# Kernel tuning notes

Measured on AMD Instinct MI355X. Metric: run time of the kernel, lower is better.

The kernel has to match this reference:

```python
import jax, jax.numpy as jnp
import numpy as np

B, LC, LQ, D = 256, 400, 50, 128
NEG = 1e12


def setup_inputs() -> dict:
    key = jax.random.key(0)
    ks = jax.random.split(key, 7)
    return {
        "x_cont": jax.random.normal(ks[0], (B, LC, D), dtype=jnp.float32),
        "x_ques": jax.random.normal(ks[1], (B, LQ, D), dtype=jnp.float32),
        "W0": jax.random.normal(ks[2], (D, 1), dtype=jnp.float32) * (1.0 / np.sqrt(D)),
        "W1": jax.random.normal(ks[3], (D, 1), dtype=jnp.float32) * (1.0 / np.sqrt(D)),
        "W2": jax.random.normal(ks[4], (1, 1, D), dtype=jnp.float32) * (1.0 / np.sqrt(D)),
        "cont_len": jax.random.randint(ks[5], (B, 1), 1, LC, dtype=jnp.int32),
        "ques_len": jax.random.randint(ks[6], (B, 1), 1, LQ, dtype=jnp.int32),
    }


def reference(x_cont, x_ques, W0, W1, W2, cont_len, ques_len):
    # Trilinear similarity S[b,c,q] = xc.W0 + xq.W1 + (xc*W2).xq
    s_c = x_cont @ W0                                   # (B, LC, 1)
    s_q = jnp.swapaxes(x_ques @ W1, 1, 2)               # (B, 1, LQ)
    s_f = jnp.einsum('bcd,bqd->bcq', x_cont * W2, x_ques)
    S = s_c + s_q + s_f                                 # (B, LC, LQ)

    # Length masks: position valid iff pos < seq_len (matches one_hot+cumsum)
    q_mask = (jnp.arange(LQ)[None, :] < ques_len).astype(S.dtype)  # (B, LQ)
    c_mask = (jnp.arange(LC)[None, :] < cont_len).astype(S.dtype)  # (B, LC)

    S_bar = jax.nn.softmax(S - (1.0 - q_mask)[:, None, :] * NEG, axis=-1)
    S_T = jnp.swapaxes(
        jax.nn.softmax(S - (1.0 - c_mask)[:, :, None] * NEG, axis=1), 1, 2)  # (B, LQ, LC)

    c2q = S_bar @ x_ques                                # (B, LC, D)
    q2c = (S_bar @ S_T) @ x_cont                        # (B, LC, D)

    result = jnp.concatenate(
        [x_cont, c2q, x_cont * c2q, x_cont * q2c], axis=-1)  # (B, LC, 4D)
    return result, S_bar, S_T
```

## Files before the change

### kernel.cpp

```cpp
#include <hip/hip_runtime.h>
#include <math.h>

#define B 256
#define LC 400
#define LQ 50
#define D 128
#define CT 64

__global__ __launch_bounds__(256) void k_scores_softmax(
    const float* __restrict__ xc_g, const float* __restrict__ xq_g,
    const float* __restrict__ W0, const float* __restrict__ W1,
    const float* __restrict__ W2, const int* __restrict__ cont_len,
    const int* __restrict__ ques_len,
    float* __restrict__ S_bar, float* __restrict__ S_T)
{
    __shared__ float sS[LC * 51];
    __shared__ __align__(16) float xq[56 * 132];
    __shared__ __align__(16) float xc[64 * 132];
    __shared__ float w[3 * D];
    __shared__ float scT[64];
    __shared__ float sq[56];
    __shared__ float rowmax[LC], rowinv[LC];
    __shared__ float colmax[LQ], colinv[LQ];
    __shared__ float red[256];

    const int b = blockIdx.x;
    const int t = threadIdx.x;
    const int clen = cont_len[b];
    const int qlen = ques_len[b];

    const float4* xq4g = (const float4*)(xq_g + (size_t)b * LQ * D);
    for (int i = t; i < LQ * 32; i += 256)
        ((float4*)xq)[(i >> 5) * 33 + (i & 31)] = xq4g[i];
    {
        const float4* g0 = (const float4*)(xc_g + (size_t)b * LC * D);
        for (int i = t; i < 64 * 32; i += 256)
            ((float4*)xc)[(i >> 5) * 33 + (i & 31)] = g0[i];
    }
    if (t < D) { w[t] = W0[t]; w[D + t] = W1[t]; w[2 * D + t] = W2[t]; }
    __syncthreads();

    if (t < LQ) {
        const float4* r = (const float4*)(xq + t * 132);
        const float4* wv = (const float4*)(w + D);
        float4 a = {0.f, 0.f, 0.f, 0.f};
#pragma unroll
        for (int d = 0; d < 32; ++d) {
            float4 u = r[d], v = wv[d];
            a.x += u.x * v.x; a.y += u.y * v.y; a.z += u.z * v.z; a.w += u.w * v.w;
        }
        sq[t] = a.x + a.y + a.z + a.w;
    }
    __syncthreads();
    for (int i = t; i < LQ * D; i += 256)
        xq[(i >> 7) * 132 + (i & 127)] *= w[2 * D + (i & 127)];
    __syncthreads();

    const int qg = t & 7;
    const int cg = (t >> 3) & 15;

    for (int tile = 0; tile < 7; ++tile) {
        const int c0 = tile * 64;
        const int nc = min(64, LC - c0);

        float4 pf[8];
        const int c0n = c0 + 64;
        const int ncn = (tile < 6) ? min(64, LC - c0n) : 0;
        const float4* gn = (const float4*)(xc_g + ((size_t)b * LC + c0n) * D);
#pragma unroll
        for (int k = 0; k < 8; ++k) {
            const int i = t + k * 256;
            if (i < ncn * 32) pf[k] = gn[i];
        }

        float acc[4][7];
        if (t < 128) {
#pragma unroll
            for (int i = 0; i < 4; ++i)
#pragma unroll
                for (int j = 0; j < 7; ++j) acc[i][j] = 0.f;
            const float4* xc4 = (const float4*)xc;
            const float4* xq4 = (const float4*)xq;
#pragma unroll 4
            for (int d4 = 0; d4 < 32; ++d4) {
                const float4 a0 = xc4[(cg + 0)  * 33 + d4];
                const float4 a1 = xc4[(cg + 16) * 33 + d4];
                const float4 a2 = xc4[(cg + 32) * 33 + d4];
                const float4 a3 = xc4[(cg + 48) * 33 + d4];
#pragma unroll
                for (int j = 0; j < 7; ++j) {
                    const float4 bq = xq4[(qg * 7 + j) * 33 + d4];
                    acc[0][j] += a0.x*bq.x + a0.y*bq.y + a0.z*bq.z + a0.w*bq.w;
                    acc[1][j] += a1.x*bq.x + a1.y*bq.y + a1.z*bq.z + a1.w*bq.w;
                    acc[2][j] += a2.x*bq.x + a2.y*bq.y + a2.z*bq.z + a2.w*bq.w;
                    acc[3][j] += a3.x*bq.x + a3.y*bq.y + a3.z*bq.z + a3.w*bq.w;
                }
            }
        } else if (t < 192) {
            const int c = t - 128;
            if (c < nc) {
                const float4* r = (const float4*)(xc + c * 132);
                const float4* wv = (const float4*)w;
                float4 a = {0.f, 0.f, 0.f, 0.f};
#pragma unroll
                for (int d = 0; d < 32; ++d) {
                    float4 u = r[d], v = wv[d];
                    a.x += u.x*v.x; a.y += u.y*v.y; a.z += u.z*v.z; a.w += u.w*v.w;
                }
                scT[c] = a.x + a.y + a.z + a.w;
            }
        }
        __syncthreads();

        if (t < 128) {
#pragma unroll
            for (int i = 0; i < 4; ++i) {
                const int c = cg + 16 * i;
                if (c < nc) {
                    const float sc_c = scT[c];
#pragma unroll
                    for (int j = 0; j < 7; ++j) {
                        const int q = qg * 7 + j;
                        if (q < LQ) sS[(c0 + c) * 51 + q] = acc[i][j] + sc_c + sq[q];
                    }
                }
            }
        }
#pragma unroll
        for (int k = 0; k < 8; ++k) {
            const int i = t + k * 256;
            if (i < ncn * 32) ((float4*)xc)[(i >> 5) * 33 + (i & 31)] = pf[k];
        }
        __syncthreads();
    }

    const int qq_ = t % LQ;
    const int r_ = t / LQ;
    if (t < 250) {
        float m = -INFINITY;
        const int ce = min((r_ + 1) * 80, clen);
        for (int c = r_ * 80; c < ce; ++c) m = fmaxf(m, sS[c * 51 + qq_]);
        red[t] = m;
    }
    __syncthreads();
    if (t < LQ) {
        float m = red[t];
#pragma unroll
        for (int rr = 1; rr < 5; ++rr) m = fmaxf(m, red[rr * LQ + t]);
        colmax[t] = m;
    }
    __syncthreads();
    if (t < 250) {
        float s = 0.f;
        const float cm = colmax[qq_];
        const int ce = min((r_ + 1) * 80, clen);
        for (int c = r_ * 80; c < ce; ++c) s += __expf(sS[c * 51 + qq_] - cm);
        red[t] = s;
    }
    __syncthreads();
    if (t < LQ) {
        float s = red[t];
#pragma unroll
        for (int rr = 1; rr < 5; ++rr) s += red[rr * LQ + t];
        colinv[t] = 1.f / s;
    }
    for (int c = t; c < LC; c += 256) {
        float m = -INFINITY;
        for (int q = 0; q < qlen; ++q) m = fmaxf(m, sS[c * 51 + q]);
        float s = 0.f;
        for (int q = 0; q < qlen; ++q) s += __expf(sS[c * 51 + q] - m);
        rowmax[c] = m;
        rowinv[c] = 1.f / s;
    }
    __syncthreads();

    float* Sb = S_bar + (size_t)b * LC * LQ;
    for (int i = t; i < LC * LQ; i += 256) {
        const int c = i / LQ, q = i - c * LQ;
        Sb[i] = (q < qlen) ? __expf(sS[c * 51 + q] - rowmax[c]) * rowinv[c] : 0.f;
    }
    float* STb = S_T + (size_t)b * LQ * LC;
    for (int i = t; i < LQ * LC; i += 256) {
        const int q = i / LC, c = i - q * LC;
        STb[i] = (c < clen) ? __expf(sS[c * 51 + q] - colmax[q]) * colinv[q] : 0.f;
    }
}

__global__ __launch_bounds__(256) void k_qc(
    const float* __restrict__ S_T, const float* __restrict__ xc_g,
    float* __restrict__ T)
{
    __shared__ __align__(16) float sT[56 * 404];

    const int b = blockIdx.x;
    const int t = threadIdx.x;
    const float4* STb4 = (const float4*)(S_T + (size_t)b * LQ * LC);
    float4* sTw = (float4*)sT;
    for (int i = t; i < LQ * 100; i += 256)
        sTw[(i / 100) * 101 + (i % 100)] = STb4[i];
    __syncthreads();

    const int d4 = t & 31, qg = t >> 5;
    float4 acc[7];
#pragma unroll
    for (int j = 0; j < 7; ++j) acc[j] = make_float4(0.f, 0.f, 0.f, 0.f);

    const float4* xcv = (const float4*)xc_g + (size_t)b * LC * 32 + d4;
    const float4* sT4 = (const float4*)sT;
    for (int c = 0; c < LC; c += 4) {
        const float4 x0 = xcv[(c + 0) * 32];
        const float4 x1 = xcv[(c + 1) * 32];
        const float4 x2 = xcv[(c + 2) * 32];
        const float4 x3 = xcv[(c + 3) * 32];
#pragma unroll
        for (int j = 0; j < 7; ++j) {
            const float4 wv = sT4[(qg * 7 + j) * 101 + (c >> 2)];
            acc[j].x += wv.x * x0.x + wv.y * x1.x + wv.z * x2.x + wv.w * x3.x;
            acc[j].y += wv.x * x0.y + wv.y * x1.y + wv.z * x2.y + wv.w * x3.y;
            acc[j].z += wv.x * x0.z + wv.y * x1.z + wv.z * x2.z + wv.w * x3.z;
            acc[j].w += wv.x * x0.w + wv.y * x1.w + wv.z * x2.w + wv.w * x3.w;
        }
    }
    float4* Tb = (float4*)T + (size_t)b * LQ * 32 + d4;
#pragma unroll
    for (int j = 0; j < 7; ++j) {
        const int qq = qg * 7 + j;
        if (qq < LQ) Tb[qq * 32] = acc[j];
    }
}

#define FMA4(A, s, V) { A.x += (s) * V.x; A.y += (s) * V.y; A.z += (s) * V.z; A.w += (s) * V.w; }

__global__ __launch_bounds__(256) void k_out(
    const float* __restrict__ S_bar, const float* __restrict__ xq_g,
    const float* __restrict__ Tm, const float* __restrict__ xc_g,
    float* __restrict__ out)
{
    __shared__ __align__(16) float xqL[LQ * 132];
    __shared__ __align__(16) float TL[LQ * 132];
    __shared__ __align__(16) float sbT[LQ * 68];

    const int b = blockIdx.y;
    const int c0 = blockIdx.x * CT;
    const int t = threadIdx.x;
    const int nc = min(CT, LC - c0);

    const float4* xq4g = (const float4*)(xq_g + (size_t)b * LQ * D);
    const float4* T4g  = (const float4*)(Tm + (size_t)b * LQ * D);
    for (int i = t; i < LQ * 32; i += 256) {
        const int row = i >> 5, col = i & 31;
        ((float4*)xqL)[row * 33 + col] = xq4g[i];
        ((float4*)TL)[row * 33 + col]  = T4g[i];
    }
    const float* sb_g = S_bar + (size_t)(b * LC + c0) * LQ;
    for (int i = t; i < nc * LQ; i += 256) {
        const int c = i / LQ, q = i - c * LQ;
        sbT[q * 68 + c] = sb_g[i];
    }
    __syncthreads();

    const int d4 = t & 31, cg = t >> 5;
    float4 c2q[8], q2c[8];
#pragma unroll
    for (int i = 0; i < 8; ++i) {
        c2q[i] = make_float4(0.f, 0.f, 0.f, 0.f);
        q2c[i] = make_float4(0.f, 0.f, 0.f, 0.f);
    }
    const float4* xq4 = (const float4*)xqL;
    const float4* T4  = (const float4*)TL;
    const float4* sb4 = (const float4*)sbT;
    const int cb2 = cg * 2;
    for (int qq = 0; qq < LQ; ++qq) {
        const float4 xv = xq4[qq * 33 + d4];
        const float4 tv = T4[qq * 33 + d4];
        const float4 s0 = sb4[qq * 17 + cb2];
        const float4 s1 = sb4[qq * 17 + cb2 + 1];
        FMA4(c2q[0], s0.x, xv); FMA4(q2c[0], s0.x, tv);
        FMA4(c2q[1], s0.y, xv); FMA4(q2c[1], s0.y, tv);
        FMA4(c2q[2], s0.z, xv); FMA4(q2c[2], s0.z, tv);
        FMA4(c2q[3], s0.w, xv); FMA4(q2c[3], s0.w, tv);
        FMA4(c2q[4], s1.x, xv); FMA4(q2c[4], s1.x, tv);
        FMA4(c2q[5], s1.y, xv); FMA4(q2c[5], s1.y, tv);
        FMA4(c2q[6], s1.z, xv); FMA4(q2c[6], s1.z, tv);
        FMA4(c2q[7], s1.w, xv); FMA4(q2c[7], s1.w, tv);
    }

    const int cbase = cg * 8;
    const float4* xcv = (const float4*)xc_g;
    float4* out4 = (float4*)out;
#pragma unroll
    for (int i = 0; i < 8; ++i) {
        const int c = cbase + i;
        if (c < nc) {
            const int row = b * LC + c0 + c;
            const float4 xc = xcv[(size_t)row * 32 + d4];
            float4* o = out4 + (size_t)row * 128 + d4;
            o[0] = xc;
            o[32] = c2q[i];
            o[64] = make_float4(xc.x * c2q[i].x, xc.y * c2q[i].y,
                                xc.z * c2q[i].z, xc.w * c2q[i].w);
            o[96] = make_float4(xc.x * q2c[i].x, xc.y * q2c[i].y,
                                xc.z * q2c[i].z, xc.w * q2c[i].w);
        }
    }
}

extern "C" void kernel_launch(void* const* d_in, const int* in_sizes, int n_in,
                              void* d_out, int out_size, void* d_ws, size_t ws_size,
                              hipStream_t stream)
{
    (void)in_sizes; (void)n_in; (void)out_size; (void)ws_size;
    const float* x_cont = (const float*)d_in[0];
    const float* x_ques = (const float*)d_in[1];
    const float* W0 = (const float*)d_in[2];
    const float* W1 = (const float*)d_in[3];
    const float* W2 = (const float*)d_in[4];
    const int* cont_len = (const int*)d_in[5];
    const int* ques_len = (const int*)d_in[6];

    float* out = (float*)d_out;
    float* out_res  = out;
    float* out_Sbar = out + (size_t)B * LC * 4 * D;
    float* out_ST   = out_Sbar + (size_t)B * LC * LQ;
    float* Tws = (float*)d_ws;

    k_scores_softmax<<<B, 256, 0, stream>>>(x_cont, x_ques, W0, W1, W2,
                                            cont_len, ques_len, out_Sbar, out_ST);
    k_qc<<<B, 256, 0, stream>>>(out_ST, x_cont, Tws);
    k_out<<<dim3(7, B), 256, 0, stream>>>(out_Sbar, x_ques, Tws, x_cont, out_res);
}
```

Measured before the change: 520.7 us.

## Split score kernel across context tiles and move column softmax into qc kernel

New measurement: 446.7 us. -14.2%, faster.

```diff
diff --git a/kernel.cpp b/kernel.cpp
--- a/kernel.cpp
+++ b/kernel.cpp
@@ -7,36 +7,31 @@
 #define D 128
 #define CT 64
 
-__global__ __launch_bounds__(256) void k_scores_softmax(
+__global__ __launch_bounds__(256) void k_scores_rowsm(
     const float* __restrict__ xc_g, const float* __restrict__ xq_g,
     const float* __restrict__ W0, const float* __restrict__ W1,
-    const float* __restrict__ W2, const int* __restrict__ cont_len,
-    const int* __restrict__ ques_len,
-    float* __restrict__ S_bar, float* __restrict__ S_T)
+    const float* __restrict__ W2, const int* __restrict__ ques_len,
+    float* __restrict__ S_bar, float* __restrict__ S_Traw)
 {
-    __shared__ float sS[LC * 51];
     __shared__ __align__(16) float xq[56 * 132];
-    __shared__ __align__(16) float xc[64 * 132];
+    __shared__ __align__(16) float xc[CT * 132];
     __shared__ float w[3 * D];
-    __shared__ float scT[64];
-    __shared__ float sq[56];
-    __shared__ float rowmax[LC], rowinv[LC];
-    __shared__ float colmax[LQ], colinv[LQ];
-    __shared__ float red[256];
-
-    const int b = blockIdx.x;
+    __shared__ float sq[56], sc[CT];
+    __shared__ float sS[CT * 51];
+    __shared__ float rowm[CT], rowi[CT];
+
+    const int b = blockIdx.y;
+    const int c0 = blockIdx.x * CT;
     const int t = threadIdx.x;
-    const int clen = cont_len[b];
+    const int nc = min(CT, LC - c0);
     const int qlen = ques_len[b];
 
     const float4* xq4g = (const float4*)(xq_g + (size_t)b * LQ * D);
     for (int i = t; i < LQ * 32; i += 256)
         ((float4*)xq)[(i >> 5) * 33 + (i & 31)] = xq4g[i];
-    {
-        const float4* g0 = (const float4*)(xc_g + (size_t)b * LC * D);
-        for (int i = t; i < 64 * 32; i += 256)
-            ((float4*)xc)[(i >> 5) * 33 + (i & 31)] = g0[i];
-    }
+    const float4* xc4g = (const float4*)(xc_g + (size_t)(b * LC + c0) * D);
+    for (int i = t; i < nc * 32; i += 256)
+        ((float4*)xc)[(i >> 5) * 33 + (i & 31)] = xc4g[i];
     if (t < D) { w[t] = W0[t]; w[D + t] = W1[t]; w[2 * D + t] = W2[t]; }
     __syncthreads();
 
@@ -50,160 +45,140 @@
             a.x += u.x * v.x; a.y += u.y * v.y; a.z += u.z * v.z; a.w += u.w * v.w;
         }
         sq[t] = a.x + a.y + a.z + a.w;
+    } else if (t >= 64 && t < 64 + CT) {
+        const int c = t - 64;
+        if (c < nc) {
+            const float4* r = (const float4*)(xc + c * 132);
+            const float4* wv = (const float4*)w;
+            float4 a = {0.f, 0.f, 0.f, 0.f};
+#pragma unroll
+            for (int d = 0; d < 32; ++d) {
+                float4 u = r[d], v = wv[d];
+                a.x += u.x * v.x; a.y += u.y * v.y; a.z += u.z * v.z; a.w += u.w * v.w;
+            }
+            sc[c] = a.x + a.y + a.z + a.w;
+        }
     }
     __syncthreads();
     for (int i = t; i < LQ * D; i += 256)
         xq[(i >> 7) * 132 + (i & 127)] *= w[2 * D + (i & 127)];
     __syncthreads();
 
-    const int qg = t & 7;
-    const int cg = (t >> 3) & 15;
-
-    for (int tile = 0; tile < 7; ++tile) {
-        const int c0 = tile * 64;
-        const int nc = min(64, LC - c0);
-
-        float4 pf[8];
-        const int c0n = c0 + 64;
-        const int ncn = (tile < 6) ? min(64, LC - c0n) : 0;
-        const float4* gn = (const float4*)(xc_g + ((size_t)b * LC + c0n) * D);
-#pragma unroll
-        for (int k = 0; k < 8; ++k) {
-            const int i = t + k * 256;
-            if (i < ncn * 32) pf[k] = gn[i];
-        }
-
-        float acc[4][7];
-        if (t < 128) {
-#pragma unroll
-            for (int i = 0; i < 4; ++i)
-#pragma unroll
-                for (int j = 0; j < 7; ++j) acc[i][j] = 0.f;
-            const float4* xc4 = (const float4*)xc;
-            const float4* xq4 = (const float4*)xq;
-#pragma unroll 4
-            for (int d4 = 0; d4 < 32; ++d4) {
-                const float4 a0 = xc4[(cg + 0)  * 33 + d4];
-                const float4 a1 = xc4[(cg + 16) * 33 + d4];
-                const float4 a2 = xc4[(cg + 32) * 33 + d4];
-                const float4 a3 = xc4[(cg + 48) * 33 + d4];
-#pragma unroll
-                for (int j = 0; j < 7; ++j) {
-                    const float4 bq = xq4[(qg * 7 + j) * 33 + d4];
-                    acc[0][j] += a0.x*bq.x + a0.y*bq.y + a0.z*bq.z + a0.w*bq.w;
-                    acc[1][j] += a1.x*bq.x + a1.y*bq.y + a1.z*bq.z + a1.w*bq.w;
-                    acc[2][j] += a2.x*bq.x + a2.y*bq.y + a2.z*bq.z + a2.w*bq.w;
-                    acc[3][j] += a3.x*bq.x + a3.y*bq.y + a3.z*bq.z + a3.w*bq.w;
-                }
+    const int qg = t & 7, cg = t >> 3;
+    const int cA = cg * 2;
+    if (cA < nc) {
+        float accA[7] = {0, 0, 0, 0, 0, 0, 0};
+        float accB[7] = {0, 0, 0, 0, 0, 0, 0};
+        const float4* xc4 = (const float4*)xc;
+        const float4* xq4 = (const float4*)xq;
+#pragma unroll 8
+        for (int d4 = 0; d4 < 32; ++d4) {
+            const float4 a0 = xc4[cA * 33 + d4];
+            const float4 a1 = xc4[(cA + 1) * 33 + d4];
+#pragma unroll
+            for (int j = 0; j < 7; ++j) {
+                const float4 bq = xq4[(qg * 7 + j) * 33 + d4];
+                accA[j] += a0.x * bq.x + a0.y * bq.y + a0.z * bq.z + a0.w * bq.w;
+                accB[j] += a1.x * bq.x + a1.y * bq.y + a1.z * bq.z + a1.w * bq.w;
             }
-        } else if (t < 192) {
-            const int c = t - 128;
-            if (c < nc) {
-                const float4* r = (const float4*)(xc + c * 132);
-                const float4* wv = (const float4*)w;
-                float4 a = {0.f, 0.f, 0.f, 0.f};
-#pragma unroll
-                for (int d = 0; d < 32; ++d) {
-                    float4 u = r[d], v = wv[d];
-                    a.x += u.x*v.x; a.y += u.y*v.y; a.z += u.z*v.z; a.w += u.w*v.w;
-                }
-                scT[c] = a.x + a.y + a.z + a.w;
+        }
+        const float scA = sc[cA], scB = sc[cA + 1];
+#pragma unroll
+        for (int j = 0; j < 7; ++j) {
+            const int q = qg * 7 + j;
+            if (q < LQ) {
+                sS[cA * 51 + q] = accA[j] + scA + sq[q];
+                sS[(cA + 1) * 51 + q] = accB[j] + scB + sq[q];
             }
         }
-        __syncthreads();
-
-        if (t < 128) {
-#pragma unroll
-            for (int i = 0; i < 4; ++i) {
-                const int c = cg + 16 * i;
-                if (c < nc) {
-                    const float sc_c = scT[c];
-#pragma unroll
-                    for (int j = 0; j < 7; ++j) {
-                        const int q = qg * 7 + j;
-                        if (q < LQ) sS[(c0 + c) * 51 + q] = acc[i][j] + sc_c + sq[q];
-                    }
-                }
-            }
-        }
-#pragma unroll
-        for (int k = 0; k < 8; ++k) {
-            const int i = t + k * 256;
-            if (i < ncn * 32) ((float4*)xc)[(i >> 5) * 33 + (i & 31)] = pf[k];
-        }
-        __syncthreads();
-    }
-
-    const int qq_ = t % LQ;
-    const int r_ = t / LQ;
+    }
+    __syncthreads();
+
+    if (t < nc) {
+        float m = -INFINITY;
+        for (int q = 0; q < qlen; ++q) m = fmaxf(m, sS[t * 51 + q]);
+        float s = 0.f;
+        for (int q = 0; q < qlen; ++q) s += __expf(sS[t * 51 + q] - m);
+        rowm[t] = m;
+        rowi[t] = 1.f / s;
+    }
+    __syncthreads();
+
+    float* Sb = S_bar + (size_t)(b * LC + c0) * LQ;
+    for (int i = t; i < nc * LQ; i += 256) {
+        const int c = i / LQ, q = i - c * LQ;
+        Sb[i] = (q < qlen) ? __expf(sS[c * 51 + q] - rowm[c]) * rowi[c] : 0.f;
+    }
+    float* STb = S_Traw + (size_t)b * LQ * LC + c0;
+    for (int i = t; i < LQ * 64; i += 256) {
+        const int q = i >> 6, c = i & 63;
+        if (c < nc) STb[q * LC + c] = sS[c * 51 + q];
+    }
+}
+
+__global__ __launch_bounds__(512) void k_colsm_qc(
+    float* __restrict__ S_T, const float* __restrict__ xc_g,
+    const int* __restrict__ cont_len, float* __restrict__ T)
+{
+    __shared__ __align__(16) float sT[56 * 404];
+    __shared__ float red[256];
+    __shared__ float colmax[LQ], colinv[LQ];
+
+    const int b = blockIdx.x;
+    const int t = threadIdx.x;
+    const int clen = cont_len[b];
+    float* STb = S_T + (size_t)b * LQ * LC;
+
+    const float4* STb4 = (const float4*)STb;
+    float4* sTw = (float4*)sT;
+    for (int i = t; i < LQ * 100; i += 512)
+        sTw[(i / 100) * 101 + (i % 100)] = STb4[i];
+    __syncthreads();
+
+    const int qr = t / 5, g = t - qr * 5;
     if (t < 250) {
         float m = -INFINITY;
-        const int ce = min((r_ + 1) * 80, clen);
-        for (int c = r_ * 80; c < ce; ++c) m = fmaxf(m, sS[c * 51 + qq_]);
+        const int ce = min((g + 1) * 80, clen);
+        for (int c = g * 80; c < ce; ++c) m = fmaxf(m, sT[qr * 404 + c]);
         red[t] = m;
     }
     __syncthreads();
     if (t < LQ) {
-        float m = red[t];
-#pragma unroll
-        for (int rr = 1; rr < 5; ++rr) m = fmaxf(m, red[rr * LQ + t]);
+        float m = red[t * 5];
+#pragma unroll
+        for (int k = 1; k < 5; ++k) m = fmaxf(m, red[t * 5 + k]);
         colmax[t] = m;
     }
     __syncthreads();
     if (t < 250) {
         float s = 0.f;
-        const float cm = colmax[qq_];
-        const int ce = min((r_ + 1) * 80, clen);
-        for (int c = r_ * 80; c < ce; ++c) s += __expf(sS[c * 51 + qq_] - cm);
+        const float cm = colmax[qr];
+        const int ce = min((g + 1) * 80, clen);
+        for (int c = g * 80; c < ce; ++c) s += __expf(sT[qr * 404 + c] - cm);
         red[t] = s;
     }
     __syncthreads();
     if (t < LQ) {
-        float s = red[t];
-#pragma unroll
-        for (int rr = 1; rr < 5; ++rr) s += red[rr * LQ + t];
+        float s = red[t * 5];
+#pragma unroll
+        for (int k = 1; k < 5; ++k) s += red[t * 5 + k];
         colinv[t] = 1.f / s;
     }
-    for (int c = t; c < LC; c += 256) {
-        float m = -INFINITY;
-        for (int q = 0; q < qlen; ++q) m = fmaxf(m, sS[c * 51 + q]);
-        float s = 0.f;
-        for (int q = 0; q < qlen; ++q) s += __expf(sS[c * 51 + q] - m);
-        rowmax[c] = m;
-        rowinv[c] = 1.f / s;
-    }
-    __syncthreads();
-
-    float* Sb = S_bar + (size_t)b * LC * LQ;
-    for (int i = t; i < LC * LQ; i += 256) {
-        const int c = i / LQ, q = i - c * LQ;
-        Sb[i] = (q < qlen) ? __expf(sS[c * 51 + q] - rowmax[c]) * rowinv[c] : 0.f;
-    }
-    float* STb = S_T + (size_t)b * LQ * LC;
-    for (int i = t; i < LQ * LC; i += 256) {
+    __syncthreads();
+
+    for (int i = t; i < LQ * LC; i += 512) {
         const int q = i / LC, c = i - q * LC;
-        STb[i] = (c < clen) ? __expf(sS[c * 51 + q] - colmax[q]) * colinv[q] : 0.f;
-    }
-}
-
-__global__ __launch_bounds__(256) void k_qc(
-    const float* __restrict__ S_T, const float* __restrict__ xc_g,
-    float* __restrict__ T)
-{
-    __shared__ __align__(16) float sT[56 * 404];
-
-    const int b = blockIdx.x;
-    const int t = threadIdx.x;
-    const float4* STb4 = (const float4*)(S_T + (size_t)b * LQ * LC);
-    float4* sTw = (float4*)sT;
-    for (int i = t; i < LQ * 100; i += 256)
-        sTw[(i / 100) * 101 + (i % 100)] = STb4[i];
+        const float v = (c < clen) ? __expf(sT[q * 404 + c] - colmax[q]) * colinv[q] : 0.f;
+        sT[q * 404 + c] = v;
+        STb[i] = v;
+    }
     __syncthreads();
 
     const int d4 = t & 31, qg = t >> 5;
-    float4 acc[7];
-#pragma unroll
-    for (int j = 0; j < 7; ++j) acc[j] = make_float4(0.f, 0.f, 0.f, 0.f);
+    const int qb = qg * 4;
+    float4 acc[4];
+#pragma unroll
+    for (int j = 0; j < 4; ++j) acc[j] = make_float4(0.f, 0.f, 0.f, 0.f);
 
     const float4* xcv = (const float4*)xc_g + (size_t)b * LC * 32 + d4;
     const float4* sT4 = (const float4*)sT;
@@ -213,8 +188,9 @@
         const float4 x2 = xcv[(c + 2) * 32];
         const float4 x3 = xcv[(c + 3) * 32];
 #pragma unroll
-        for (int j = 0; j < 7; ++j) {
-            const float4 wv = sT4[(qg * 7 + j) * 101 + (c >> 2)];
+        for (int j = 0; j < 4; ++j) {
+            const int q = min(qb + j, LQ - 1);
+            const float4 wv = sT4[q * 101 + (c >> 2)];
             acc[j].x += wv.x * x0.x + wv.y * x1.x + wv.z * x2.x + wv.w * x3.x;
             acc[j].y += wv.x * x0.y + wv.y * x1.y + wv.z * x2.y + wv.w * x3.y;
             acc[j].z += wv.x * x0.z + wv.y * x1.z + wv.z * x2.z + wv.w * x3.z;
@@ -223,9 +199,9 @@
     }
     float4* Tb = (float4*)T + (size_t)b * LQ * 32 + d4;
 #pragma unroll
-    for (int j = 0; j < 7; ++j) {
-        const int qq = qg * 7 + j;
-        if (qq < LQ) Tb[qq * 32] = acc[j];
+    for (int j = 0; j < 4; ++j) {
+        const int q = qb + j;
+        if (q < LQ) Tb[q * 32] = acc[j];
     }
 }
 
@@ -324,8 +300,8 @@
     float* out_ST   = out_Sbar + (size_t)B * LC * LQ;
     float* Tws = (float*)d_ws;
 
-    k_scores_softmax<<<B, 256, 0, stream>>>(x_cont, x_ques, W0, W1, W2,
-                                            cont_len, ques_len, out_Sbar, out_ST);
-    k_qc<<<B, 256, 0, stream>>>(out_ST, x_cont, Tws);
+    k_scores_rowsm<<<dim3(7, B), 256, 0, stream>>>(x_cont, x_ques, W0, W1, W2,
+                                                   ques_len, out_Sbar, out_ST);
+    k_colsm_qc<<<B, 512, 0, stream>>>(out_ST, x_cont, cont_len, Tws);
     k_out<<<dim3(7, B), 256, 0, stream>>>(out_Sbar, x_ques, Tws, x_cont, out_res);
 }
```
